# Optimization experiments

Measured on AMD Instinct MI355X. Metric: run time of the kernel, lower is better.

Reference implementation:

```python
import jax, jax.numpy as jnp
import numpy as np

B, T, D, H = 2, 2048, 1024, 16
DK = D // H


def setup_inputs() -> dict:
    key = jax.random.key(0)
    ks = jax.random.split(key, 12)
    s = 1.0 / np.sqrt(D)
    inp = {
        "q_inp": jax.random.normal(ks[0], (B, T, D), jnp.float32),
        "k_inp": jax.random.normal(ks[1], (B, T, D), jnp.float32),
        "v_inp": jax.random.normal(ks[2], (B, T, D), jnp.float32),
        # causal mask: True = position is masked out
        "attn_mask": jnp.triu(jnp.ones((T, T), jnp.bool_), k=1),
        "Wq": jax.random.uniform(ks[3], (D, D), jnp.float32, -s, s),
        "bq": jax.random.uniform(ks[4], (D,), jnp.float32, -s, s),
        "Wk": jax.random.uniform(ks[5], (D, D), jnp.float32, -s, s),
        "bk": jax.random.uniform(ks[6], (D,), jnp.float32, -s, s),
        "Wv": jax.random.uniform(ks[7], (D, D), jnp.float32, -s, s),
        "bv": jax.random.uniform(ks[8], (D,), jnp.float32, -s, s),
        "Wo": jax.random.uniform(ks[9], (D, D), jnp.float32, -s, s),
        "bo": jax.random.uniform(ks[10], (D,), jnp.float32, -s, s),
    }
    return inp


def _split_heads(x):
    # [B,T,D] -> [B,H,T,DK]
    Bx, Tx, _ = x.shape
    return x.reshape(Bx, Tx, H, DK).transpose(0, 2, 1, 3)


def reference(q_inp, k_inp, v_inp, attn_mask, Wq, bq, Wk, bk, Wv, bv, Wo, bo):
    Q = _split_heads(q_inp @ Wq + bq)
    K = _split_heads(k_inp @ Wk + bk)
    V = _split_heads(v_inp @ Wv + bv)
    scale = 1.0 / jnp.sqrt(jnp.asarray(DK, Q.dtype))
    scores = jnp.einsum("bhqd,bhkd->bhqk", Q, K) * scale  # [B,H,T,T]
    scores = jnp.where(attn_mask, -jnp.inf, scores)
    attn = jax.nn.softmax(scores, axis=-1)  # dropout p=0 -> identity
    ctx = jnp.einsum("bhqk,bhkd->bhqd", attn, V)
    out = ctx.transpose(0, 2, 1, 3).reshape(B, T, D) @ Wo + bo
    return (out, attn)
```

## Files before the change

kernel.cpp:

```cpp
#include <hip/hip_runtime.h>
#include <hip/hip_bf16.h>
#include <math.h>


typedef unsigned short bfu;
typedef __attribute__((ext_vector_type(8))) short short8;
typedef __attribute__((ext_vector_type(4))) float f32x4;

#define AS1(p) ((const __attribute__((address_space(1))) void*)(p))
#define AS3(p) ((__attribute__((address_space(3))) void*)(p))
#define SOFT_C 16.0f

__device__ __forceinline__ void gld16(const void* g, void* l) {
  __builtin_amdgcn_global_load_lds(AS1(g), AS3(l), 16, 0, 0);
}

__device__ __forceinline__ bfu f2bf(float f) {
  unsigned int u = __float_as_uint(f);
  u = (u + 0x7fffu + ((u >> 16) & 1u)) >> 16;
  return (bfu)u;
}
__device__ __forceinline__ float bf2f(bfu b) {
  return __uint_as_float(((unsigned int)b) << 16);
}
__device__ __forceinline__ short8 lds_read8(const bfu* p) {
  return *reinterpret_cast<const short8*>(p);
}

__global__ __launch_bounds__(256) void cvt_x_kernel(
    const float* __restrict__ q, const float* __restrict__ k,
    const float* __restrict__ v, bfu* __restrict__ out) {
  size_t idx = ((size_t)blockIdx.x * 256 + threadIdx.x) * 8;
  const float* src; size_t off;
  if (idx < 4194304u)       { src = q; off = idx; }
  else if (idx < 8388608u)  { src = k; off = idx - 4194304u; }
  else                      { src = v; off = idx - 8388608u; }
  float4 a = *reinterpret_cast<const float4*>(src + off);
  float4 b = *reinterpret_cast<const float4*>(src + off + 4);
  short8 r;
  r[0] = (short)f2bf(a.x); r[1] = (short)f2bf(a.y);
  r[2] = (short)f2bf(a.z); r[3] = (short)f2bf(a.w);
  r[4] = (short)f2bf(b.x); r[5] = (short)f2bf(b.y);
  r[6] = (short)f2bf(b.z); r[7] = (short)f2bf(b.w);
  *reinterpret_cast<short8*>(out + idx) = r;
}

__global__ __launch_bounds__(256) void cvt_wt_kernel(
    const float* __restrict__ Wq, const float* __restrict__ Wk,
    const float* __restrict__ Wv, const float* __restrict__ Wo,
    bfu* __restrict__ Wt) {
  __shared__ float tile[32][33];
  const int z = blockIdx.z;
  const float* W = z == 0 ? Wq : z == 1 ? Wk : z == 2 ? Wv : Wo;
  bfu* out = Wt + (size_t)z * 1048576;
  const int n0 = blockIdx.x * 32, k0 = blockIdx.y * 32;
  const int tx = threadIdx.x, ty = threadIdx.y;
#pragma unroll
  for (int i = 0; i < 4; ++i)
    tile[ty + i * 8][tx] = W[(size_t)(k0 + ty + i * 8) * 1024 + n0 + tx];
  __syncthreads();
#pragma unroll
  for (int i = 0; i < 4; ++i)
    out[(size_t)(n0 + ty + i * 8) * 1024 + k0 + tx] = f2bf(tile[tx][ty + i * 8]);
}

template <int MODE>
__global__ __launch_bounds__(256, 2) void gemm_bt_kernel(
    const bfu* __restrict__ Aall, const bfu* __restrict__ Btall,
    const float* __restrict__ bias0, const float* __restrict__ bias1,
    const float* __restrict__ bias2, bfu* __restrict__ outQKV,
    float* __restrict__ outF) {
  __shared__ bfu sA[128 * 64];
  __shared__ bfu sB[128 * 64];
  const int z = blockIdx.z;
  const int m0 = blockIdx.x * 128, n0 = blockIdx.y * 128;
  const bfu* A = Aall + (size_t)z * 4194304;
  const bfu* Bt = Btall + (size_t)z * 1048576;
  const float* bias = (z == 0) ? bias0 : (z == 1 ? bias1 : bias2);
  const int tid = threadIdx.x, w = tid >> 6, l = tid & 63;
  const int quad = l >> 4, lane16 = l & 15;
  const int l7 = lane16 & 7;
  const int mb = (w >> 1) * 64, nb = (w & 1) * 64;

  f32x4 acc[4][4] = {};

  for (int kt = 0; kt < 16; ++kt) {
    const int k0 = kt * 64;
    __syncthreads();
#pragma unroll
    for (int j = 0; j < 4; ++j) {
      const int chunk = (w * 4 + j) * 64 + l;
      const int row = chunk >> 3, c = (chunk & 7) ^ (row & 7);
      gld16(A + (size_t)(m0 + row) * 1024 + k0 + c * 8, sA + chunk * 8);
      gld16(Bt + (size_t)(n0 + row) * 1024 + k0 + c * 8, sB + chunk * 8);
    }
    __syncthreads();
#pragma unroll
    for (int ks = 0; ks < 2; ++ks) {
      const int cf = ((ks * 4 + quad) ^ l7) * 8;
      short8 af[4], bfr[4];
#pragma unroll
      for (int x = 0; x < 4; ++x) {
        af[x]  = lds_read8(sA + (mb + x * 16 + lane16) * 64 + cf);
        bfr[x] = lds_read8(sB + (nb + x * 16 + lane16) * 64 + cf);
      }
#pragma unroll
      for (int mi = 0; mi < 4; ++mi)
#pragma unroll
        for (int ni = 0; ni < 4; ++ni)
          acc[mi][ni] = __builtin_amdgcn_mfma_f32_16x16x32_bf16(
              af[mi], bfr[ni], acc[mi][ni], 0, 0, 0);
    }
  }

#pragma unroll
  for (int ni = 0; ni < 4; ++ni) {
    const int n = n0 + nb + ni * 16 + lane16;
    const float bv = bias[n];
#pragma unroll
    for (int mi = 0; mi < 4; ++mi) {
#pragma unroll
      for (int r = 0; r < 4; ++r) {
        const int m = m0 + mb + mi * 16 + quad * 4 + r;
        float v = acc[mi][ni][r] + bv;
        if (MODE == 0) {
          if (z == 0) v *= 0.125f;
          const int b = m >> 11, t = m & 2047;
          const int h = n >> 6, dk = n & 63;
          outQKV[(size_t)z * 4194304 +
                 (((size_t)(b * 16 + h) * 2048 + t) * 64 + dk)] = f2bf(v);
        } else {
          outF[(size_t)m * 1024 + n] = v;
        }
      }
    }
  }
}

__global__ __launch_bounds__(256) void vt_kernel(const bfu* __restrict__ V,
                                                 bfu* __restrict__ vT) {
  __shared__ bfu sT[64][72];
  const int bh = blockIdx.y, t0 = blockIdx.x * 64;
  const int tid = threadIdx.x;
  const bfu* src = V + (size_t)bh * 131072 + (size_t)t0 * 64;
#pragma unroll
  for (int j = 0; j < 2; ++j) {
    const int ch = j * 256 + tid;
    const int row = ch >> 3, c = ch & 7;
    short8 v = *reinterpret_cast<const short8*>(src + row * 64 + c * 8);
#pragma unroll
    for (int e = 0; e < 8; ++e) sT[c * 8 + e][row] = (bfu)v[e];
  }
  __syncthreads();
#pragma unroll
  for (int j = 0; j < 2; ++j) {
    const int ch = j * 256 + tid;
    const int d = ch >> 3, c = ch & 7;
    short8 o = lds_read8(&sT[d][c * 8]);
    *reinterpret_cast<short8*>(vT + (size_t)bh * 131072 + (size_t)d * 2048 +
                               t0 + c * 8) = o;
  }
}

__global__ __launch_bounds__(256, 2) void attn_kernel(
    const bfu* __restrict__ qkv, const bfu* __restrict__ vT,
    float* __restrict__ attnO, bfu* __restrict__ ctx) {
  __shared__ bfu sQ[128 * 64];
  __shared__ bfu sK[64 * 64];
  __shared__ bfu sVt[64 * 64];
  __shared__ bfu sP[128 * 72];
  const int bh = blockIdx.y;
  const int iq = (bh & 16) ? (int)blockIdx.x : 15 - (int)blockIdx.x;
  const int tid = threadIdx.x, w = tid >> 6, l = tid & 63;
  const int quad = l >> 4, lane16 = l & 15;
  const int l7 = lane16 & 7;
  const bfu* Qb = qkv + ((size_t)bh * 2048 + iq * 128) * 64;
  const bfu* Kb = qkv + 4194304 + (size_t)bh * 131072;
  const bfu* VTb = vT + (size_t)bh * 131072;
  float* attnRow = attnO + (size_t)bh * 4194304 + (size_t)iq * 128 * 2048;

#pragma unroll
  for (int j = 0; j < 4; ++j) {
    const int chunk = (w * 4 + j) * 64 + l;
    const int row = chunk >> 3, c = (chunk & 7) ^ (row & 7);
    gld16(Qb + row * 64 + c * 8, sQ + chunk * 8);
  }

  const int jmax = 2 * iq + 1;
  const int wrow0 = iq * 128 + w * 32;
  const int jmaxw = (wrow0 + 31) >> 6;

  float esum[2][4] = {};

  for (int jj = 0; jj <= jmax; ++jj) {
    __syncthreads();
#pragma unroll
    for (int j = 0; j < 2; ++j) {
      const int chunk = (w * 2 + j) * 64 + l;
      const int row = chunk >> 3, c = (chunk & 7) ^ (row & 7);
      gld16(Kb + (size_t)jj * 4096 + row * 64 + c * 8, sK + chunk * 8);
    }
    __syncthreads();
    if (jj <= jmaxw) {
      f32x4 s[2][4] = {};
#pragma unroll
      for (int ks = 0; ks < 2; ++ks) {
        const int cf = ((ks * 4 + quad) ^ l7) * 8;
        short8 aq[2], kb[4];
        aq[0] = lds_read8(sQ + (w * 32 + lane16) * 64 + cf);
        aq[1] = lds_read8(sQ + (w * 32 + 16 + lane16) * 64 + cf);
#pragma unroll
        for (int nf = 0; nf < 4; ++nf)
          kb[nf] = lds_read8(sK + (nf * 16 + lane16) * 64 + cf);
#pragma unroll
        for (int mf = 0; mf < 2; ++mf)
#pragma unroll
          for (int nf = 0; nf < 4; ++nf)
            s[mf][nf] = __builtin_amdgcn_mfma_f32_16x16x32_bf16(
                aq[mf], kb[nf], s[mf][nf], 0, 0, 0);
      }
      if (jj * 64 + 63 > wrow0) {
#pragma unroll
        for (int mf = 0; mf < 2; ++mf)
#pragma unroll
          for (int nf = 0; nf < 4; ++nf)
#pragma unroll
            for (int r = 0; r < 4; ++r) {
              const int qg = wrow0 + mf * 16 + quad * 4 + r;
              const int kg = jj * 64 + nf * 16 + lane16;
              if (kg > qg) s[mf][nf][r] = -INFINITY;
            }
      }
#pragma unroll
      for (int mf = 0; mf < 2; ++mf)
#pragma unroll
        for (int r = 0; r < 4; ++r) {
          float a = __expf(s[mf][0][r] - SOFT_C) + __expf(s[mf][1][r] - SOFT_C);
          float b = __expf(s[mf][2][r] - SOFT_C) + __expf(s[mf][3][r] - SOFT_C);
          esum[mf][r] += a + b;
        }
    }
  }
  float linv[2][4];
#pragma unroll
  for (int mf = 0; mf < 2; ++mf)
#pragma unroll
    for (int r = 0; r < 4; ++r) {
      float e = esum[mf][r];
      e += __shfl_xor(e, 1, 64);
      e += __shfl_xor(e, 2, 64);
      e += __shfl_xor(e, 4, 64);
      e += __shfl_xor(e, 8, 64);
      linv[mf][r] = 1.f / e;
    }

  f32x4 o[2][4] = {};
  for (int jj = 0; jj <= jmax; ++jj) {
    __syncthreads();
#pragma unroll
    for (int j = 0; j < 2; ++j) {
      const int chunk = (w * 2 + j) * 64 + l;
      const int row = chunk >> 3, c = (chunk & 7) ^ (row & 7);
      gld16(Kb + (size_t)jj * 4096 + row * 64 + c * 8, sK + chunk * 8);
      gld16(VTb + (size_t)row * 2048 + jj * 64 + c * 8, sVt + chunk * 8);
    }
    __syncthreads();
    if (jj <= jmaxw) {
      f32x4 s[2][4] = {};
#pragma unroll
      for (int ks = 0; ks < 2; ++ks) {
        const int cf = ((ks * 4 + quad) ^ l7) * 8;
        short8 aq[2], kb[4];
        aq[0] = lds_read8(sQ + (w * 32 + lane16) * 64 + cf);
        aq[1] = lds_read8(sQ + (w * 32 + 16 + lane16) * 64 + cf);
#pragma unroll
        for (int nf = 0; nf < 4; ++nf)
          kb[nf] = lds_read8(sK + (nf * 16 + lane16) * 64 + cf);
#pragma unroll
        for (int mf = 0; mf < 2; ++mf)
#pragma unroll
          for (int nf = 0; nf < 4; ++nf)
            s[mf][nf] = __builtin_amdgcn_mfma_f32_16x16x32_bf16(
                aq[mf], kb[nf], s[mf][nf], 0, 0, 0);
      }
      if (jj * 64 + 63 > wrow0) {
#pragma unroll
        for (int mf = 0; mf < 2; ++mf)
#pragma unroll
          for (int nf = 0; nf < 4; ++nf)
#pragma unroll
            for (int r = 0; r < 4; ++r) {
              const int qg = wrow0 + mf * 16 + quad * 4 + r;
              const int kg = jj * 64 + nf * 16 + lane16;
              if (kg > qg) s[mf][nf][r] = -INFINITY;
            }
      }
#pragma unroll
      for (int mf = 0; mf < 2; ++mf)
#pragma unroll
        for (int nf = 0; nf < 4; ++nf)
#pragma unroll
          for (int r = 0; r < 4; ++r) {
            const float p = __expf(s[mf][nf][r] - SOFT_C) * linv[mf][r];
            sP[(w * 32 + mf * 16 + quad * 4 + r) * 72 + nf * 16 + lane16] =
                f2bf(p);
          }
#pragma unroll
      for (int ks = 0; ks < 2; ++ks) {
        const int cf = ((ks * 4 + quad) ^ l7) * 8;
        short8 ap[2], vb[4];
        ap[0] = lds_read8(sP + (w * 32 + lane16) * 72 + ks * 32 + quad * 8);
        ap[1] = lds_read8(sP + (w * 32 + 16 + lane16) * 72 + ks * 32 + quad * 8);
#pragma unroll
        for (int nf = 0; nf < 4; ++nf)
          vb[nf] = lds_read8(sVt + (nf * 16 + lane16) * 64 + cf);
#pragma unroll
        for (int mf = 0; mf < 2; ++mf)
#pragma unroll
          for (int nf = 0; nf < 4; ++nf)
            o[mf][nf] = __builtin_amdgcn_mfma_f32_16x16x32_bf16(
                ap[mf], vb[nf], o[mf][nf], 0, 0, 0);
      }
#pragma unroll
      for (int it = 0; it < 4; ++it) {
        const int lin = it * 64 + l;
        const int row = lin >> 3, ch = (lin & 7) * 8;
        short8 pv = lds_read8(sP + (w * 32 + row) * 72 + ch);
        float4 f0, f1;
        f0.x = bf2f((bfu)pv[0]); f0.y = bf2f((bfu)pv[1]);
        f0.z = bf2f((bfu)pv[2]); f0.w = bf2f((bfu)pv[3]);
        f1.x = bf2f((bfu)pv[4]); f1.y = bf2f((bfu)pv[5]);
        f1.z = bf2f((bfu)pv[6]); f1.w = bf2f((bfu)pv[7]);
        float* gp = attnRow + (size_t)(w * 32 + row) * 2048 + jj * 64 + ch;
        *reinterpret_cast<float4*>(gp) = f0;
        *reinterpret_cast<float4*>(gp + 4) = f1;
      }
    }
  }

  {
    const int colz = (jmaxw + 1) * 64;
    const int nz4 = (2048 - colz) >> 2;
    const float4 z4 = {0.f, 0.f, 0.f, 0.f};
    for (int r = 0; r < 32; ++r) {
      float* rp = attnRow + (size_t)(w * 32 + r) * 2048 + colz;
      for (int c = l; c < nz4; c += 64) reinterpret_cast<float4*>(rp)[c] = z4;
    }
  }

  __syncthreads();
#pragma unroll
  for (int mf = 0; mf < 2; ++mf)
#pragma unroll
    for (int nf = 0; nf < 4; ++nf)
#pragma unroll
      for (int r = 0; r < 4; ++r)
        sP[(w * 32 + mf * 16 + quad * 4 + r) * 72 + nf * 16 + lane16] =
            f2bf(o[mf][nf][r]);
  __syncthreads();
  const int b = bh >> 4, h = bh & 15;
#pragma unroll
  for (int it = 0; it < 4; ++it) {
    const int lin = it * 256 + tid;
    const int row = lin >> 3, ch = (lin & 7) * 8;
    short8 v = lds_read8(sP + row * 72 + ch);
    *reinterpret_cast<short8*>(
        ctx + ((size_t)(b * 2048 + iq * 128 + row)) * 1024 + h * 64 + ch) = v;
  }
}

extern "C" void kernel_launch(void* const* d_in, const int* in_sizes, int n_in,
                              void* d_out, int out_size, void* d_ws,
                              size_t ws_size, hipStream_t stream) {
  const float* q_inp = (const float*)d_in[0];
  const float* k_inp = (const float*)d_in[1];
  const float* v_inp = (const float*)d_in[2];
  const float* Wq = (const float*)d_in[4];
  const float* bq = (const float*)d_in[5];
  const float* Wk = (const float*)d_in[6];
  const float* bk = (const float*)d_in[7];
  const float* Wv = (const float*)d_in[8];
  const float* bv = (const float*)d_in[9];
  const float* Wo = (const float*)d_in[10];
  const float* bo = (const float*)d_in[11];

  bfu* X   = (bfu*)d_ws;
  bfu* Wt  = X + 12582912;
  bfu* qkv = Wt + 4194304;
  bfu* ctx = qkv + 12582912;
  bfu* vT  = X;
  float* out  = (float*)d_out;
  float* attn = out + 4194304;

  cvt_x_kernel<<<6144, 256, 0, stream>>>(q_inp, k_inp, v_inp, X);
  cvt_wt_kernel<<<dim3(32, 32, 4), dim3(32, 8), 0, stream>>>(Wq, Wk, Wv, Wo, Wt);
  gemm_bt_kernel<0><<<dim3(32, 8, 3), 256, 0, stream>>>(X, Wt, bq, bk, bv, qkv,
                                                        nullptr);
  vt_kernel<<<dim3(32, 32), 256, 0, stream>>>(qkv + 8388608, vT);
  attn_kernel<<<dim3(16, 32), 256, 0, stream>>>(qkv, vT, attn, ctx);
  gemm_bt_kernel<1><<<dim3(32, 8, 1), 256, 0, stream>>>(ctx, Wt + 3 * 1048576,
                                                        bo, bo, bo, nullptr, out);
}
```

Baseline: 741.1 us.

## Double-buffer K/V tiles in attention, keep Q fragments in registers

The K and V^T shared-memory tiles become double-buffered, so the next tile's async global-to-LDS load is issued before computing on the current one, and each iteration needs one barrier instead of two. Q fragments are loaded once from global memory straight into registers instead of staged in LDS, which frees LDS and removes repeated LDS reads. s_setprio brackets raise wave priority around the MFMA sections. The cost is more LDS for the doubled buffers and more registers held for Q, which could pressure occupancy under launch_bounds(256,2).

```diff
diff --git a/kernel.cpp b/kernel.cpp
--- a/kernel.cpp
+++ b/kernel.cpp
@@ -165,9 +165,8 @@
 __global__ __launch_bounds__(256, 2) void attn_kernel(
     const bfu* __restrict__ qkv, const bfu* __restrict__ vT,
     float* __restrict__ attnO, bfu* __restrict__ ctx) {
-  __shared__ bfu sQ[128 * 64];
-  __shared__ bfu sK[64 * 64];
-  __shared__ bfu sVt[64 * 64];
+  __shared__ bfu sK[2][64 * 64];
+  __shared__ bfu sVt[2][64 * 64];
   __shared__ bfu sP[128 * 72];
   const int bh = blockIdx.y;
   const int iq = (bh & 16) ? (int)blockIdx.x : 15 - (int)blockIdx.x;
@@ -179,12 +178,13 @@
   const bfu* VTb = vT + (size_t)bh * 131072;
   float* attnRow = attnO + (size_t)bh * 4194304 + (size_t)iq * 128 * 2048;
 
-#pragma unroll
-  for (int j = 0; j < 4; ++j) {
-    const int chunk = (w * 4 + j) * 64 + l;
-    const int row = chunk >> 3, c = (chunk & 7) ^ (row & 7);
-    gld16(Qb + row * 64 + c * 8, sQ + chunk * 8);
-  }
+  short8 aq[2][2];
+#pragma unroll
+  for (int mf = 0; mf < 2; ++mf)
+#pragma unroll
+    for (int ks = 0; ks < 2; ++ks)
+      aq[mf][ks] = *reinterpret_cast<const short8*>(
+          Qb + (size_t)(w * 32 + mf * 16 + lane16) * 64 + (ks * 4 + quad) * 8);
 
   const int jmax = 2 * iq + 1;
   const int wrow0 = iq * 128 + w * 32;
@@ -192,33 +192,42 @@
 
   float esum[2][4] = {};
 
+#pragma unroll
+  for (int j = 0; j < 2; ++j) {
+    const int chunk = (w * 2 + j) * 64 + l;
+    const int row = chunk >> 3, c = (chunk & 7) ^ (row & 7);
+    gld16(Kb + row * 64 + c * 8, sK[0] + chunk * 8);
+  }
+  __syncthreads();
+  int cur = 0;
   for (int jj = 0; jj <= jmax; ++jj) {
-    __syncthreads();
-#pragma unroll
-    for (int j = 0; j < 2; ++j) {
-      const int chunk = (w * 2 + j) * 64 + l;
-      const int row = chunk >> 3, c = (chunk & 7) ^ (row & 7);
-      gld16(Kb + (size_t)jj * 4096 + row * 64 + c * 8, sK + chunk * 8);
-    }
-    __syncthreads();
+    if (jj < jmax) {
+#pragma unroll
+      for (int j = 0; j < 2; ++j) {
+        const int chunk = (w * 2 + j) * 64 + l;
+        const int row = chunk >> 3, c = (chunk & 7) ^ (row & 7);
+        gld16(Kb + (size_t)(jj + 1) * 4096 + row * 64 + c * 8,
+              sK[cur ^ 1] + chunk * 8);
+      }
+    }
     if (jj <= jmaxw) {
       f32x4 s[2][4] = {};
+      __builtin_amdgcn_s_setprio(1);
 #pragma unroll
       for (int ks = 0; ks < 2; ++ks) {
         const int cf = ((ks * 4 + quad) ^ l7) * 8;
-        short8 aq[2], kb[4];
-        aq[0] = lds_read8(sQ + (w * 32 + lane16) * 64 + cf);
-        aq[1] = lds_read8(sQ + (w * 32 + 16 + lane16) * 64 + cf);
+        short8 kb[4];
 #pragma unroll
         for (int nf = 0; nf < 4; ++nf)
-          kb[nf] = lds_read8(sK + (nf * 16 + lane16) * 64 + cf);
+          kb[nf] = lds_read8(sK[cur] + (nf * 16 + lane16) * 64 + cf);
 #pragma unroll
         for (int mf = 0; mf < 2; ++mf)
 #pragma unroll
           for (int nf = 0; nf < 4; ++nf)
             s[mf][nf] = __builtin_amdgcn_mfma_f32_16x16x32_bf16(
-                aq[mf], kb[nf], s[mf][nf], 0, 0, 0);
-      }
+                aq[mf][ks], kb[nf], s[mf][nf], 0, 0, 0);
+      }
+      __builtin_amdgcn_s_setprio(0);
       if (jj * 64 + 63 > wrow0) {
 #pragma unroll
         for (int mf = 0; mf < 2; ++mf)
@@ -240,6 +249,8 @@
           esum[mf][r] += a + b;
         }
     }
+    __syncthreads();
+    cur ^= 1;
   }
   float linv[2][4];
 #pragma unroll
@@ -255,34 +266,45 @@
     }
 
   f32x4 o[2][4] = {};
+#pragma unroll
+  for (int j = 0; j < 2; ++j) {
+    const int chunk = (w * 2 + j) * 64 + l;
+    const int row = chunk >> 3, c = (chunk & 7) ^ (row & 7);
+    gld16(Kb + row * 64 + c * 8, sK[0] + chunk * 8);
+    gld16(VTb + (size_t)row * 2048 + c * 8, sVt[0] + chunk * 8);
+  }
+  __syncthreads();
+  cur = 0;
   for (int jj = 0; jj <= jmax; ++jj) {
-    __syncthreads();
-#pragma unroll
-    for (int j = 0; j < 2; ++j) {
-      const int chunk = (w * 2 + j) * 64 + l;
-      const int row = chunk >> 3, c = (chunk & 7) ^ (row & 7);
-      gld16(Kb + (size_t)jj * 4096 + row * 64 + c * 8, sK + chunk * 8);
-      gld16(VTb + (size_t)row * 2048 + jj * 64 + c * 8, sVt + chunk * 8);
-    }
-    __syncthreads();
+    if (jj < jmax) {
+#pragma unroll
+      for (int j = 0; j < 2; ++j) {
+        const int chunk = (w * 2 + j) * 64 + l;
+        const int row = chunk >> 3, c = (chunk & 7) ^ (row & 7);
+        gld16(Kb + (size_t)(jj + 1) * 4096 + row * 64 + c * 8,
+              sK[cur ^ 1] + chunk * 8);
+        gld16(VTb + (size_t)row * 2048 + (jj + 1) * 64 + c * 8,
+              sVt[cur ^ 1] + chunk * 8);
+      }
+    }
     if (jj <= jmaxw) {
       f32x4 s[2][4] = {};
+      __builtin_amdgcn_s_setprio(1);
 #pragma unroll
       for (int ks = 0; ks < 2; ++ks) {
         const int cf = ((ks * 4 + quad) ^ l7) * 8;
-        short8 aq[2], kb[4];
-        aq[0] = lds_read8(sQ + (w * 32 + lane16) * 64 + cf);
-        aq[1] = lds_read8(sQ + (w * 32 + 16 + lane16) * 64 + cf);
+        short8 kb[4];
 #pragma unroll
         for (int nf = 0; nf < 4; ++nf)
-          kb[nf] = lds_read8(sK + (nf * 16 + lane16) * 64 + cf);
+          kb[nf] = lds_read8(sK[cur] + (nf * 16 + lane16) * 64 + cf);
 #pragma unroll
         for (int mf = 0; mf < 2; ++mf)
 #pragma unroll
           for (int nf = 0; nf < 4; ++nf)
             s[mf][nf] = __builtin_amdgcn_mfma_f32_16x16x32_bf16(
-                aq[mf], kb[nf], s[mf][nf], 0, 0, 0);
-      }
+                aq[mf][ks], kb[nf], s[mf][nf], 0, 0, 0);
+      }
+      __builtin_amdgcn_s_setprio(0);
       if (jj * 64 + 63 > wrow0) {
 #pragma unroll
         for (int mf = 0; mf < 2; ++mf)
@@ -305,6 +327,7 @@
             sP[(w * 32 + mf * 16 + quad * 4 + r) * 72 + nf * 16 + lane16] =
                 f2bf(p);
           }
+      __builtin_amdgcn_s_setprio(1);
 #pragma unroll
       for (int ks = 0; ks < 2; ++ks) {
         const int cf = ((ks * 4 + quad) ^ l7) * 8;
@@ -313,7 +336,7 @@
         ap[1] = lds_read8(sP + (w * 32 + 16 + lane16) * 72 + ks * 32 + quad * 8);
 #pragma unroll
         for (int nf = 0; nf < 4; ++nf)
-          vb[nf] = lds_read8(sVt + (nf * 16 + lane16) * 64 + cf);
+          vb[nf] = lds_read8(sVt[cur] + (nf * 16 + lane16) * 64 + cf);
 #pragma unroll
         for (int mf = 0; mf < 2; ++mf)
 #pragma unroll
@@ -321,6 +344,7 @@
             o[mf][nf] = __builtin_amdgcn_mfma_f32_16x16x32_bf16(
                 ap[mf], vb[nf], o[mf][nf], 0, 0, 0);
       }
+      __builtin_amdgcn_s_setprio(0);
 #pragma unroll
       for (int it = 0; it < 4; ++it) {
         const int lin = it * 64 + l;
@@ -336,6 +360,8 @@
         *reinterpret_cast<float4*>(gp + 4) = f1;
       }
     }
+    __syncthreads();
+    cur ^= 1;
   }
 
   {
```

Result: no change. 737.2 us (-0.5%).
